# Kernel tuning notes

Measured on AMD Instinct MI355X. Metric: run time of the kernel, lower is better.

The kernel has to match this reference:

```python
import jax, jax.numpy as jnp
import numpy as np

N_STEPS = 2048  # forward arg `n`: number of recurrence steps


def setup_inputs() -> dict:
    key = jax.random.key(0)
    kx, k2, k3, kb, k4 = jax.random.split(key, 5)
    x = jax.random.normal(kx, (5,), dtype=jnp.float32)
    # scalar weights of the 1x1 Linears; kept small so the 2047-step
    # recurrence (factor 1 - w2^2 - w4^2) stays numerically stable
    w2 = jax.random.uniform(k2, (), jnp.float32, -0.3, 0.3)  # lambda2.weight
    w3 = jax.random.uniform(k3, (), jnp.float32, -0.3, 0.3)  # lambda3.weight
    b3 = jax.random.uniform(kb, (), jnp.float32, -0.3, 0.3)  # lambda3.bias
    w4 = jax.random.uniform(k4, (), jnp.float32, -0.3, 0.3)  # lambda4.weight
    return {"x": x, "w2": w2, "w3": w3, "b3": b3, "w4": w4, "n": N_STEPS}


def reference(x, w2, w3, b3, w4, n):
    # Faithful SIR recurrence. In the torch module, ns[i] starts as zeros(5)
    # and only slots 0..3 are written, so slot 4 is 0 for every step i >= 1.
    x = x.reshape(5)

    def step(s, _):
        s0, s1, s2, s3 = s[0], s[1], s[2], s[3]
        a = w2 * (w2 * s0)                              # lambda2(lambda2(s0))
        b = w4 * (w4 * s0)                              # lambda4(lambda4(s0))
        c = w3 * (w3 * (s0 / 1000.0 * s2) + b3) + b3    # lambda3(lambda3(s0/1000*s2))
        new = jnp.stack([s0 - a - b + c, s1 + a, s2 - c, s3 + b,
                         jnp.zeros_like(s0)])
        return new, new

    _, ys = jax.lax.scan(step, x, None, length=n - 1)
    return ys  # (n-1, 5): rows ns[1]..ns[n-1] concatenated, as in torch
```

## Files before the change

kernel.cpp:

```cpp
#include <hip/hip_runtime.h>


typedef float f2 __attribute__((ext_vector_type(2)));

#define STEP(Wv, FGv)                                                    \
  asm("v_pk_fma_f32 %0, %1, %2, %3 op_sel:[0,1,0] op_sel_hi:[1,0,1]"     \
      : "=v"(FGv) : "v"(C1), "v"(Wv), "v"(C2));                          \
  asm("v_pk_fma_f32 %0, %0, %1, %2" : "+v"(Wv) : "v"(FGv), "v"(C3));

template <int CTRL, int RMASK>
__device__ __forceinline__ float dpp0(float x) {
  return __int_as_float(__builtin_amdgcn_update_dpp(
      0, __float_as_int(x), CTRL, RMASK, 0xf, false));
}

__device__ __forceinline__ float wave_incl_scan(float x) {
  x += dpp0<0x111, 0xf>(x);
  x += dpp0<0x112, 0xf>(x);
  x += dpp0<0x114, 0xf>(x);
  x += dpp0<0x118, 0xf>(x);
  x += dpp0<0x142, 0xa>(x);
  x += dpp0<0x143, 0xc>(x);
  return x;
}

__global__ __launch_bounds__(64) void sir_kernel(
    const float* __restrict__ x, const float* __restrict__ w2p,
    const float* __restrict__ w3p, const float* __restrict__ b3p,
    const float* __restrict__ w4p, const int* __restrict__ np,
    float* __restrict__ out) {
  const int lane = threadIdx.x;
  const int n = *np;
  const int rows = n - 1;

  const float w2 = *w2p, w3 = *w3p, b3 = *b3p, w4 = *w4p;
  const float w2sq  = w2 * w2;
  const float w4sq  = w4 * w4;
  const float L     = 1.0f - w2sq - w4sq;
  const float gamma = (w3 * w3) / 1000.0f;
  const float delta = fmaf(w3, b3, b3);
  const float s1_0 = x[1], s3_0 = x[3];

  if (rows == 2047) {
    f2 W;  W.x = x[0];  W.y = x[2];
    f2 C1; C1.x = gamma; C1.y = -gamma;
    f2 C2; C2.x = L;     C2.y = 1.0f;
    f2 C3; C3.x = delta; C3.y = -delta;

    float G = W.x;

#pragma unroll 1
    for (int b = 0; b < 4; ++b) {
      float PU = 0.0f, PV = 0.0f;
#pragma unroll
      for (int jj = 0; jj < 64; ++jj) {
        f2 FG;
        STEP(W, FG)
        const bool park = (lane == jj);
        PU = park ? W.x : PU;
        PV = park ? W.y : PV;
#pragma unroll
        for (int t = 1; t < 8; ++t) { f2 FG2; STEP(W, FG2) }
      }
      float U[8], V[8];
      f2 R; R.x = PU; R.y = PV;
      U[0] = PU; V[0] = PV;
#pragma unroll
      for (int t = 1; t < 8; ++t) { f2 FG; STEP(R, FG) U[t] = R.x; V[t] = R.y; }
      float Q = U[0];
#pragma unroll
      for (int t = 1; t < 8; ++t) Q += U[t];
      const float S = wave_incl_scan(Q);
      float T = G + (S - Q);
      G += __shfl(S, 63);
      float flat[40];
#pragma unroll
      for (int t = 0; t < 8; ++t) {
        flat[5 * t + 0] = U[t];
        flat[5 * t + 1] = fmaf(w2sq, T, s1_0);
        flat[5 * t + 2] = V[t];
        flat[5 * t + 3] = fmaf(w4sq, T, s3_0);
        flat[5 * t + 4] = 0.0f;
        T += U[t];
      }
      float4* __restrict__ q4 = (float4*)(out + 2560 * b + 40 * lane);
      if (b < 3 || lane < 63) {
#pragma unroll
        for (int k = 0; k < 10; ++k)
          q4[k] = make_float4(flat[4*k], flat[4*k+1], flat[4*k+2], flat[4*k+3]);
      } else {
#pragma unroll
        for (int k = 0; k < 8; ++k)
          q4[k] = make_float4(flat[4*k], flat[4*k+1], flat[4*k+2], flat[4*k+3]);
        ((float2*)(q4 + 8))[0] = make_float2(flat[32], flat[33]);
        ((float*)q4)[34] = flat[34];
      }
    }
  } else {
    if (lane == 0) {
      float u = x[0], v = x[2], s1 = s1_0, s3 = s3_0;
      const float mgamma = -gamma, mdelta = -delta;
      float* __restrict__ p = out;
#pragma unroll 4
      for (int i = 0; i < rows; ++i) {
        const float f = fmaf(gamma, v, L);
        const float g = fmaf(mgamma, u, 1.0f);
        s1 = fmaf(w2sq, u, s1);
        s3 = fmaf(w4sq, u, s3);
        u = fmaf(u, f, delta);
        v = fmaf(v, g, mdelta);
        p[0] = u; p[1] = s1; p[2] = v; p[3] = s3; p[4] = 0.0f;
        p += 5;
      }
    }
  }
}

extern "C" void kernel_launch(void* const* d_in, const int* in_sizes, int n_in,
                              void* d_out, int out_size, void* d_ws, size_t ws_size,
                              hipStream_t stream) {
  const float* x   = (const float*)d_in[0];
  const float* w2  = (const float*)d_in[1];
  const float* w3  = (const float*)d_in[2];
  const float* b3  = (const float*)d_in[3];
  const float* w4  = (const float*)d_in[4];
  const int*   n   = (const int*)d_in[5];
  float* out = (float*)d_out;
  sir_kernel<<<1, 64, 0, stream>>>(x, w2, w3, b3, w4, n, out);
}
```

Baseline: 80.09 us.

## Checkpoint serial chain to LDS and expand outputs across two waves

One wave now runs the full serial recurrence and stores a state checkpoint every 16 steps into shared memory, without the per-lane parking selects the old loop needed. After a barrier, 128 threads each restart from their own checkpoint, recompute 16 steps and write 80 output floats. The earlier four sequential block epilogues, each with its own scan and store phase, become a single parallel epilogue spread over two waves. The cost is an LDS round trip, two barriers and a cross-wave prefix carry passed through shared memory.

New measurement: 79.59 us. About the same (-0.6%).

```diff
diff --git a/kernel.cpp b/kernel.cpp
--- a/kernel.cpp
+++ b/kernel.cpp
@@ -24,12 +24,12 @@
   return x;
 }
 
-__global__ __launch_bounds__(64) void sir_kernel(
+__global__ __launch_bounds__(128) void sir_kernel(
     const float* __restrict__ x, const float* __restrict__ w2p,
     const float* __restrict__ w3p, const float* __restrict__ b3p,
     const float* __restrict__ w4p, const int* __restrict__ np,
     float* __restrict__ out) {
-  const int lane = threadIdx.x;
+  const int tid = threadIdx.x;
   const int n = *np;
   const int rows = n - 1;
 
@@ -41,50 +41,58 @@
   const float delta = fmaf(w3, b3, b3);
   const float s1_0 = x[1], s3_0 = x[3];
 
+  f2 C1; C1.x = gamma; C1.y = -gamma;
+  f2 C2; C2.x = L;     C2.y = 1.0f;
+  f2 C3; C3.x = delta; C3.y = -delta;
+
   if (rows == 2047) {
-    f2 W;  W.x = x[0];  W.y = x[2];
-    f2 C1; C1.x = gamma; C1.y = -gamma;
-    f2 C2; C2.x = L;     C2.y = 1.0f;
-    f2 C3; C3.x = delta; C3.y = -delta;
+    __shared__ f2 ck[128][64];
+    __shared__ float tot;
 
-    float G = W.x;
+    if (tid < 64) {
+      f2 W; W.x = x[0]; W.y = x[2];
+#pragma unroll 1
+      for (int b = 0; b < 8; ++b) {
+#pragma unroll
+        for (int i = 0; i < 16; ++i) {
+          ck[b * 16 + i][tid] = W;
+#pragma unroll
+          for (int t = 0; t < 16; ++t) { f2 FG; STEP(W, FG) }
+        }
+      }
+    }
+    __syncthreads();
 
-#pragma unroll 1
-    for (int b = 0; b < 4; ++b) {
-      float PU = 0.0f, PV = 0.0f;
+    const int g = tid;
+    f2 R = ck[g][g & 63];
+    float U[17], V[17];
+    U[0] = R.x; V[0] = R.y;
 #pragma unroll
-      for (int jj = 0; jj < 64; ++jj) {
-        f2 FG;
-        STEP(W, FG)
-        const bool park = (lane == jj);
-        PU = park ? W.x : PU;
-        PV = park ? W.y : PV;
+    for (int t = 1; t <= 16; ++t) { f2 FG; STEP(R, FG) U[t] = R.x; V[t] = R.y; }
+
+    float Q = U[0];
 #pragma unroll
-        for (int t = 1; t < 8; ++t) { f2 FG2; STEP(W, FG2) }
-      }
-      float U[8], V[8];
-      f2 R; R.x = PU; R.y = PV;
-      U[0] = PU; V[0] = PV;
+    for (int t = 1; t < 16; ++t) Q += U[t];
+    const float S = wave_incl_scan(Q);
+    if (tid == 63) tot = S;
+    __syncthreads();
+    float T = (S - Q) + (tid >= 64 ? tot : 0.0f);
+
 #pragma unroll
-      for (int t = 1; t < 8; ++t) { f2 FG; STEP(R, FG) U[t] = R.x; V[t] = R.y; }
-      float Q = U[0];
-#pragma unroll
-      for (int t = 1; t < 8; ++t) Q += U[t];
-      const float S = wave_incl_scan(Q);
-      float T = G + (S - Q);
-      G += __shfl(S, 63);
+    for (int h = 0; h < 2; ++h) {
       float flat[40];
 #pragma unroll
-      for (int t = 0; t < 8; ++t) {
-        flat[5 * t + 0] = U[t];
-        flat[5 * t + 1] = fmaf(w2sq, T, s1_0);
-        flat[5 * t + 2] = V[t];
-        flat[5 * t + 3] = fmaf(w4sq, T, s3_0);
-        flat[5 * t + 4] = 0.0f;
+      for (int t8 = 0; t8 < 8; ++t8) {
+        const int t = 8 * h + t8;
         T += U[t];
+        flat[5 * t8 + 0] = U[t + 1];
+        flat[5 * t8 + 1] = fmaf(w2sq, T, s1_0);
+        flat[5 * t8 + 2] = V[t + 1];
+        flat[5 * t8 + 3] = fmaf(w4sq, T, s3_0);
+        flat[5 * t8 + 4] = 0.0f;
       }
-      float4* __restrict__ q4 = (float4*)(out + 2560 * b + 40 * lane);
-      if (b < 3 || lane < 63) {
+      float4* __restrict__ q4 = (float4*)(out + 80 * g + 40 * h);
+      if (g < 127 || h == 0) {
 #pragma unroll
         for (int k = 0; k < 10; ++k)
           q4[k] = make_float4(flat[4*k], flat[4*k+1], flat[4*k+2], flat[4*k+3]);
@@ -97,18 +105,18 @@
       }
     }
   } else {
-    if (lane == 0) {
+    if (tid == 0) {
       float u = x[0], v = x[2], s1 = s1_0, s3 = s3_0;
       const float mgamma = -gamma, mdelta = -delta;
       float* __restrict__ p = out;
 #pragma unroll 4
       for (int i = 0; i < rows; ++i) {
         const float f = fmaf(gamma, v, L);
-        const float g = fmaf(mgamma, u, 1.0f);
+        const float gg = fmaf(mgamma, u, 1.0f);
         s1 = fmaf(w2sq, u, s1);
         s3 = fmaf(w4sq, u, s3);
         u = fmaf(u, f, delta);
-        v = fmaf(v, g, mdelta);
+        v = fmaf(v, gg, mdelta);
         p[0] = u; p[1] = s1; p[2] = v; p[3] = s3; p[4] = 0.0f;
         p += 5;
       }
@@ -126,5 +134,5 @@
   const float* w4  = (const float*)d_in[4];
   const int*   n   = (const int*)d_in[5];
   float* out = (float*)d_out;
-  sir_kernel<<<1, 64, 0, stream>>>(x, w2, w3, b3, w4, n, out);
+  sir_kernel<<<1, 128, 0, stream>>>(x, w2, w3, b3, w4, n, out);
 }
```
